# Performance work log

Hardware: AMD Instinct MI355X
Metric: run time of the kernel (lower is better)

The kernel has to match this reference:

```python
import jax, jax.numpy as jnp
import numpy as np

B, S, E, H = 4, 2048, 1024, 16
D = E // H  # head_dim = 64
MASK_VALUE = -10000.0


def setup_inputs() -> dict:
    key = jax.random.key(0)
    k1, k2, k3 = jax.random.split(key, 3)
    scale_qkv = 1.0 / np.sqrt(E)
    scale_out = 1.0 / np.sqrt(E)
    return {
        "x": jax.random.normal(k1, (B, S, E), dtype=jnp.float32),
        "w_qkv": jax.random.normal(k2, (E, 3 * E), dtype=jnp.float32) * scale_qkv,
        "b_qkv": jnp.zeros((3 * E,), dtype=jnp.float32),
        "w_out": jax.random.normal(k3, (E, E), dtype=jnp.float32) * scale_out,
        "b_out": jnp.zeros((E,), dtype=jnp.float32),
    }


def reference(x, w_qkv, b_qkv, w_out, b_out):
    # QKV projection (Dense with bias), then split into q, k, v
    qkv = x @ w_qkv + b_qkv                      # [B, S, 3E]
    q, k, v = jnp.split(qkv, 3, axis=2)          # each [B, S, E]

    def split_heads(t):
        return t.reshape(B, S, H, D).transpose(0, 2, 1, 3)  # [B, H, S, D]

    q, k, v = split_heads(q), split_heads(k), split_heads(v)

    # Scaled dot-product attention with causal mask (query_len == key_len == S)
    scores = jnp.einsum("bhqd,bhkd->bhqk", q, k) / jnp.sqrt(jnp.asarray(D, q.dtype))
    causal = jnp.tril(jnp.ones((S, S), dtype=bool))[None, None]  # [1,1,S,S]
    scores = jnp.where(causal, scores, MASK_VALUE)
    attn_weights = jax.nn.softmax(scores, axis=-1)               # [B,H,S,S]
    # attn dropout is deterministic (training=False) -> identity
    out = jnp.einsum("bhqk,bhkd->bhqd", attn_weights, v)         # [B,H,S,D]

    # Merge heads and output projection; resid dropout deterministic -> identity
    out = out.transpose(0, 2, 1, 3).reshape(B, S, E)
    out = out @ w_out + b_out
    return (out, attn_weights)
```

## Files before the change

### kernel.cpp

```cpp
#include <hip/hip_runtime.h>
#include <math.h>

typedef __attribute__((ext_vector_type(4))) float  f32x4;
typedef __attribute__((ext_vector_type(8))) __bf16 bf16x8;
typedef __attribute__((ext_vector_type(4))) __bf16 bf16x4;

constexpr int B_ = 4, S_ = 2048, E_ = 1024, H_ = 16, D_ = 64;
constexpr int M_ = B_ * S_;
constexpr int N3 = 3 * E_;

__device__ __forceinline__ f32x4 mfma16(bf16x8 a, bf16x8 b, f32x4 c) {
    return __builtin_amdgcn_mfma_f32_16x16x32_bf16(a, b, c, 0, 0, 0);
}
__device__ __forceinline__ void split2(float x, __bf16& h, __bf16& l) {
    h = (__bf16)x;
    l = (__bf16)(x - (float)h);
}

__device__ __forceinline__ void gemm_tile_core(
    const float* __restrict__ A, int lda,
    const float* __restrict__ Bm, int ldb,
    int K,
    __bf16* Ahi, __bf16* Alo, __bf16* Bhi, __bf16* Blo,
    f32x4 acc[4][4])
{
    const int tid  = threadIdx.x;
    const int lane = tid & 63;
    const int w    = tid >> 6;
    const int lr   = lane & 15;
    const int lq   = lane >> 4;
    const int wm   = w >> 1, wn = w & 1;

    for (int k0 = 0; k0 < K; k0 += 32) {
        __syncthreads();
#pragma unroll
        for (int i = 0; i < 2; ++i) {
            const int slot = tid + 256 * i;
            const int lr2 = slot & 15;
            const int lq2 = (slot >> 4) & 3;
            const int mi  = slot >> 6;
            const float* ap = A + (size_t)(mi * 16 + lr2) * lda + k0 + lq2 * 8;
            float4 a0 = *reinterpret_cast<const float4*>(ap);
            float4 a1 = *reinterpret_cast<const float4*>(ap + 4);
            float v8[8] = {a0.x, a0.y, a0.z, a0.w, a1.x, a1.y, a1.z, a1.w};
            bf16x8 hv, lv;
#pragma unroll
            for (int j = 0; j < 8; ++j) {
                __bf16 h0, l0;
                split2(v8[j], h0, l0);
                hv[j] = h0; lv[j] = l0;
            }
            *reinterpret_cast<bf16x8*>(Ahi + slot * 8) = hv;
            *reinterpret_cast<bf16x8*>(Alo + slot * 8) = lv;
        }
#pragma unroll
        for (int i = 0; i < 2; ++i) {
            const int slot = tid + 256 * i;
            const int lr2 = slot & 15;
            const int lq2 = (slot >> 4) & 3;
            const int ni  = slot >> 6;
            const float* bp = Bm + (size_t)(k0 + lq2 * 8) * ldb + ni * 16 + lr2;
            bf16x8 hv, lv;
#pragma unroll
            for (int j = 0; j < 8; ++j) {
                __bf16 h0, l0;
                split2(bp[(size_t)j * ldb], h0, l0);
                hv[j] = h0; lv[j] = l0;
            }
            *reinterpret_cast<bf16x8*>(Bhi + slot * 8) = hv;
            *reinterpret_cast<bf16x8*>(Blo + slot * 8) = lv;
        }
        __syncthreads();

        bf16x8 ah[4], al[4], bh[4], bl[4];
#pragma unroll
        for (int t = 0; t < 4; ++t) {
            const int sa = ((wm * 4 + t) * 4 + lq) * 16 + lr;
            ah[t] = *reinterpret_cast<const bf16x8*>(Ahi + sa * 8);
            al[t] = *reinterpret_cast<const bf16x8*>(Alo + sa * 8);
            const int sb = ((wn * 4 + t) * 4 + lq) * 16 + lr;
            bh[t] = *reinterpret_cast<const bf16x8*>(Bhi + sb * 8);
            bl[t] = *reinterpret_cast<const bf16x8*>(Blo + sb * 8);
        }
#pragma unroll
        for (int mi = 0; mi < 4; ++mi)
#pragma unroll
            for (int ni = 0; ni < 4; ++ni) {
                acc[mi][ni] = mfma16(ah[mi], bh[ni], acc[mi][ni]);
                acc[mi][ni] = mfma16(al[mi], bh[ni], acc[mi][ni]);
                acc[mi][ni] = mfma16(ah[mi], bl[ni], acc[mi][ni]);
            }
    }
}

__global__ __launch_bounds__(256, 2)
void qkv_kernel(const float* __restrict__ x, const float* __restrict__ wq,
                const float* __restrict__ bias,
                float* __restrict__ Qb, float* __restrict__ Kb,
                float* __restrict__ Vb) {
    __shared__ __align__(16) __bf16 Ahi[4096], Alo[4096];
    __shared__ __align__(16) __bf16 Bhi[4096], Blo[4096];

    const int bn = blockIdx.x * 128;
    const int bm = blockIdx.y * 128;
    const int tid  = threadIdx.x;
    const int lane = tid & 63;
    const int w    = tid >> 6;
    const int lr   = lane & 15;
    const int lq   = lane >> 4;
    const int wm   = w >> 1, wn = w & 1;

    f32x4 acc[4][4];
#pragma unroll
    for (int mi = 0; mi < 4; ++mi)
#pragma unroll
        for (int ni = 0; ni < 4; ++ni) acc[mi][ni] = (f32x4){0.f, 0.f, 0.f, 0.f};

    gemm_tile_core(x + (size_t)bm * E_, E_, wq + bn, N3, E_,
                   Ahi, Alo, Bhi, Blo, acc);

#pragma unroll
    for (int ni = 0; ni < 4; ++ni) {
        const int col  = bn + (wn * 4 + ni) * 16 + lr;
        const int t    = col >> 10;
        const int hcol = col & 1023;
        const int h    = hcol >> 6;
        const int d    = hcol & 63;
        float* dst = (t == 0) ? Qb : (t == 1) ? Kb : Vb;
        const float bv = bias[col];
#pragma unroll
        for (int mi = 0; mi < 4; ++mi) {
#pragma unroll
            for (int r = 0; r < 4; ++r) {
                const int row = bm + (wm * 4 + mi) * 16 + lq * 4 + r;
                const int b = row >> 11;
                const int s = row & 2047;
                dst[(((size_t)(b * H_ + h)) * S_ + s) * D_ + d] =
                    acc[mi][ni][r] + bv;
            }
        }
    }
}

__device__ __forceinline__ void stage_K(const float* __restrict__ src,
                                        __bf16* Khi, __bf16* Klo, int tid) {
    const int r0   = tid >> 4;
    const int c4   = (tid & 15) * 4;
    const int slot = (tid & 15) >> 1;
    const int half = (tid & 15) & 1;
#pragma unroll
    for (int i = 0; i < 4; ++i) {
        const int row = r0 + 16 * i;
        float4 v = *reinterpret_cast<const float4*>(&src[row * 64 + c4]);
        const int slotp = slot ^ (row & 7);
        const int idx = row * 64 + slotp * 8 + half * 4;
        bf16x4 hv, lv;
        __bf16 h0, l0;
        split2(v.x, h0, l0); hv[0] = h0; lv[0] = l0;
        split2(v.y, h0, l0); hv[1] = h0; lv[1] = l0;
        split2(v.z, h0, l0); hv[2] = h0; lv[2] = l0;
        split2(v.w, h0, l0); hv[3] = h0; lv[3] = l0;
        *reinterpret_cast<bf16x4*>(Khi + idx) = hv;
        *reinterpret_cast<bf16x4*>(Klo + idx) = lv;
    }
}

__device__ __forceinline__ void stage_V(const float* __restrict__ src,
                                        __bf16* Vhi, __bf16* Vlo, int tid) {
    const int kb  = tid >> 4;
    const int dq  = (tid & 15) * 4;
    const int kg  = kb >> 1;
    const int kc0 = (kb & 1) * 4;
    float rv[16];
#pragma unroll
    for (int i = 0; i < 4; ++i) {
        float4 t = *reinterpret_cast<const float4*>(&src[(kb * 4 + i) * 64 + dq]);
        rv[i * 4 + 0] = t.x; rv[i * 4 + 1] = t.y;
        rv[i * 4 + 2] = t.z; rv[i * 4 + 3] = t.w;
    }
#pragma unroll
    for (int di = 0; di < 4; ++di) {
        bf16x4 hv, lv;
        __bf16 h0, l0;
        split2(rv[0 * 4 + di], h0, l0); hv[0] = h0; lv[0] = l0;
        split2(rv[1 * 4 + di], h0, l0); hv[1] = h0; lv[1] = l0;
        split2(rv[2 * 4 + di], h0, l0); hv[2] = h0; lv[2] = l0;
        split2(rv[3 * 4 + di], h0, l0); hv[3] = h0; lv[3] = l0;
        const int idx = (kg * 64 + (dq + di)) * 8 + kc0;
        *reinterpret_cast<bf16x4*>(Vhi + idx) = hv;
        *reinterpret_cast<bf16x4*>(Vlo + idx) = lv;
    }
}

__device__ __forceinline__ void qk_tile(const __bf16* Khi, const __bf16* Klo,
                                        const bf16x8* qh, const bf16x8* ql,
                                        int lr, int lq, bool diag,
                                        int qrow0, int k0, f32x4 lg[4]) {
#pragma unroll
    for (int s = 0; s < 4; ++s) {
        f32x4 a = {0.f, 0.f, 0.f, 0.f};
        const int row = 16 * s + lr;
#pragma unroll
        for (int c = 0; c < 2; ++c) {
            const int slotp = (4 * c + lq) ^ (row & 7);
            bf16x8 kh = *reinterpret_cast<const bf16x8*>(Khi + row * 64 + slotp * 8);
            bf16x8 kl = *reinterpret_cast<const bf16x8*>(Klo + row * 64 + slotp * 8);
            a = mfma16(qh[c], kh, a);
            a = mfma16(ql[c], kh, a);
            a = mfma16(qh[c], kl, a);
        }
#pragma unroll
        for (int r = 0; r < 4; ++r) {
            float v = a[r] * 0.125f;
            if (diag && (k0 + 16 * s + lr) > (qrow0 + lq * 4 + r)) v = -1e30f;
            lg[s][r] = v;
        }
    }
}

__global__ __launch_bounds__(256, 3)
void attn_kernel(const float* __restrict__ Qg, const float* __restrict__ Kg,
                 const float* __restrict__ Vg, float* __restrict__ wts,
                 float* __restrict__ ctx) {
    __shared__ __align__(16) __bf16 Khi[4096];
    __shared__ __align__(16) __bf16 Klo[4096];
    __shared__ __align__(16) __bf16 Vhi[4096];
    __shared__ __align__(16) __bf16 Vlo[4096];
    __shared__ float sc[64][68];

    const int qt = blockIdx.x, h = blockIdx.y, b = blockIdx.z;
    const int q0 = qt * 64;
    const int tid = threadIdx.x;
    const int lane = tid & 63;
    const int w  = tid >> 6;
    const int lr = lane & 15;
    const int lq = lane >> 4;

    const size_t headbase = (size_t)(b * H_ + h) * S_ * D_;
    const float* Qp = Qg + headbase;
    const float* Kp = Kg + headbase;
    const float* Vp = Vg + headbase;
    float* wrow = wts + ((size_t)(b * H_ + h) * S_ + q0) * S_;

    bf16x8 qh[2], ql[2];
    {
        const int qrow = q0 + 16 * w + lr;
#pragma unroll
        for (int c = 0; c < 2; ++c) {
            const float* qp = &Qp[(size_t)qrow * D_ + c * 32 + lq * 8];
            float4 a  = *reinterpret_cast<const float4*>(qp);
            float4 bq = *reinterpret_cast<const float4*>(qp + 4);
            float v8[8] = {a.x, a.y, a.z, a.w, bq.x, bq.y, bq.z, bq.w};
#pragma unroll
            for (int j = 0; j < 8; ++j) {
                __bf16 h0, l0;
                split2(v8[j], h0, l0);
                qh[c][j] = h0; ql[c][j] = l0;
            }
        }
    }

    const int nkt = qt + 1;
    const int qrow0 = q0 + 16 * w;

    float m_run[4], l_run[4];
#pragma unroll
    for (int r = 0; r < 4; ++r) { m_run[r] = -INFINITY; l_run[r] = 0.f; }

    for (int kt = 0; kt < nkt; ++kt) {
        __syncthreads();
        stage_K(&Kp[(size_t)kt * 4096], Khi, Klo, tid);
        __syncthreads();
        f32x4 lg[4];
        qk_tile(Khi, Klo, qh, ql, lr, lq, kt == qt, qrow0, kt * 64, lg);
#pragma unroll
        for (int r = 0; r < 4; ++r) {
            float mx = fmaxf(fmaxf(lg[0][r], lg[1][r]), fmaxf(lg[2][r], lg[3][r]));
            mx = fmaxf(mx, __shfl_xor(mx, 1));
            mx = fmaxf(mx, __shfl_xor(mx, 2));
            mx = fmaxf(mx, __shfl_xor(mx, 4));
            mx = fmaxf(mx, __shfl_xor(mx, 8));
            const float mnew = fmaxf(m_run[r], mx);
            float ps = __expf(lg[0][r] - mnew) + __expf(lg[1][r] - mnew) +
                       __expf(lg[2][r] - mnew) + __expf(lg[3][r] - mnew);
            ps += __shfl_xor(ps, 1);
            ps += __shfl_xor(ps, 2);
            ps += __shfl_xor(ps, 4);
            ps += __shfl_xor(ps, 8);
            l_run[r] = l_run[r] * __expf(m_run[r] - mnew) + ps;
            m_run[r] = mnew;
        }
    }

    float linv[4];
#pragma unroll
    for (int r = 0; r < 4; ++r) linv[r] = 1.0f / l_run[r];

    f32x4 acc[4];
#pragma unroll
    for (int s = 0; s < 4; ++s) acc[s] = (f32x4){0.f, 0.f, 0.f, 0.f};

    for (int kt = 0; kt < nkt; ++kt) {
        __syncthreads();
        stage_K(&Kp[(size_t)kt * 4096], Khi, Klo, tid);
        stage_V(&Vp[(size_t)kt * 4096], Vhi, Vlo, tid);
        __syncthreads();

        f32x4 lg[4];
        qk_tile(Khi, Klo, qh, ql, lr, lq, kt == qt, qrow0, kt * 64, lg);
#pragma unroll
        for (int s = 0; s < 4; ++s)
#pragma unroll
            for (int r = 0; r < 4; ++r)
                sc[16 * w + lq * 4 + r][16 * s + lr] =
                    __expf(lg[s][r] - m_run[r]) * linv[r];
        __syncthreads();

        {
            const int c4 = (tid & 15) * 4;
            const int r0 = tid >> 4;
#pragma unroll
            for (int i = 0; i < 4; ++i) {
                const int row = r0 + 16 * i;
                float4 w4 = *reinterpret_cast<const float4*>(&sc[row][c4]);
                *reinterpret_cast<float4*>(
                    &wrow[(size_t)row * S_ + kt * 64 + c4]) = w4;
            }
        }

        bf16x8 pah[2], pal[2];
#pragma unroll
        for (int c = 0; c < 2; ++c) {
            const float* pr = &sc[16 * w + lr][lq * 8 + 32 * c];
            float4 p0 = *reinterpret_cast<const float4*>(pr);
            float4 p1 = *reinterpret_cast<const float4*>(pr + 4);
            float v8[8] = {p0.x, p0.y, p0.z, p0.w, p1.x, p1.y, p1.z, p1.w};
#pragma unroll
            for (int j = 0; j < 8; ++j) {
                __bf16 h0, l0;
                split2(v8[j], h0, l0);
                pah[c][j] = h0; pal[c][j] = l0;
            }
        }

#pragma unroll
        for (int s2 = 0; s2 < 4; ++s2) {
#pragma unroll
            for (int c = 0; c < 2; ++c) {
                const int kg = 4 * c + lq;
                const int d  = 16 * s2 + lr;
                bf16x8 vh = *reinterpret_cast<const bf16x8*>(Vhi + (kg * 64 + d) * 8);
                bf16x8 vl = *reinterpret_cast<const bf16x8*>(Vlo + (kg * 64 + d) * 8);
                acc[s2] = mfma16(pah[c], vh, acc[s2]);
                acc[s2] = mfma16(pah[c], vl, acc[s2]);
                acc[s2] = mfma16(pal[c], vh, acc[s2]);
            }
        }
    }

    {
        float4 z = {0.f, 0.f, 0.f, 0.f};
        const int c4 = (tid & 15) * 4;
        const int r0 = tid >> 4;
        for (int kt = nkt; kt < S_ / 64; ++kt) {
#pragma unroll
            for (int i = 0; i < 4; ++i) {
                const int row = r0 + 16 * i;
                *reinterpret_cast<float4*>(
                    &wrow[(size_t)row * S_ + kt * 64 + c4]) = z;
            }
        }
    }

#pragma unroll
    for (int s2 = 0; s2 < 4; ++s2)
#pragma unroll
        for (int r = 0; r < 4; ++r)
            ctx[((size_t)b * S_ + qrow0 + lq * 4 + r) * E_ + h * 64 + 16 * s2 + lr] =
                acc[s2][r];
}

__global__ __launch_bounds__(256, 2)
void proj_kernel(const float* __restrict__ ctx, const float* __restrict__ wo,
                 const float* __restrict__ bias, float* __restrict__ out) {
    __shared__ __align__(16) __bf16 Ahi[4096], Alo[4096];
    __shared__ __align__(16) __bf16 Bhi[4096], Blo[4096];

    const int bn = blockIdx.x * 128;
    const int bm = blockIdx.y * 128;
    const int tid  = threadIdx.x;
    const int lane = tid & 63;
    const int w    = tid >> 6;
    const int lr   = lane & 15;
    const int lq   = lane >> 4;
    const int wm   = w >> 1, wn = w & 1;

    f32x4 acc[4][4];
#pragma unroll
    for (int mi = 0; mi < 4; ++mi)
#pragma unroll
        for (int ni = 0; ni < 4; ++ni) acc[mi][ni] = (f32x4){0.f, 0.f, 0.f, 0.f};

    gemm_tile_core(ctx + (size_t)bm * E_, E_, wo + bn, E_, E_,
                   Ahi, Alo, Bhi, Blo, acc);

#pragma unroll
    for (int ni = 0; ni < 4; ++ni) {
        const int col = bn + (wn * 4 + ni) * 16 + lr;
        const float bv = bias[col];
#pragma unroll
        for (int mi = 0; mi < 4; ++mi) {
#pragma unroll
            for (int r = 0; r < 4; ++r) {
                const int row = bm + (wm * 4 + mi) * 16 + lq * 4 + r;
                out[(size_t)row * E_ + col] = acc[mi][ni][r] + bv;
            }
        }
    }
}

extern "C" void kernel_launch(void* const* d_in, const int* in_sizes, int n_in,
                              void* d_out, int out_size, void* d_ws,
                              size_t ws_size, hipStream_t stream) {
    (void)in_sizes; (void)n_in; (void)out_size; (void)ws_size;
    const float* x     = (const float*)d_in[0];
    const float* w_qkv = (const float*)d_in[1];
    const float* b_qkv = (const float*)d_in[2];
    const float* w_out = (const float*)d_in[3];
    const float* b_out = (const float*)d_in[4];

    float* out = (float*)d_out;
    float* wts = out + (size_t)M_ * E_;

    const size_t per = (size_t)B_ * H_ * S_ * D_;
    float* Qb  = (float*)d_ws;
    float* Kb  = Qb + per;
    float* Vb  = Kb + per;
    float* ctx = Vb + per;

    qkv_kernel<<<dim3(N3 / 128, M_ / 128), 256, 0, stream>>>(
        x, w_qkv, b_qkv, Qb, Kb, Vb);
    attn_kernel<<<dim3(S_ / 64, H_, B_), 256, 0, stream>>>(
        Qb, Kb, Vb, wts, ctx);
    proj_kernel<<<dim3(E_ / 128, M_ / 128), 256, 0, stream>>>(
        ctx, w_out, b_out, out);
}
```

Baseline: 1.730 ms.

## Pre-pack GEMM operands into tiled bf16 hi/lo buffers before the projection GEMMs

Adds separate pack kernels that split the fp32 activations and weights into bf16 hi/lo parts once, stored in the tile-ordered layout the MFMA loop reads. The QKV and output-projection GEMMs then copy contiguous pre-split tiles into shared memory instead of converting fp32 inside every block. Before, each A tile was re-split by every column block, and the B loads were strided column reads. In exchange the change adds four extra launches and extra global traffic for the packed buffers. The output-projection packed buffers reuse the Q workspace, which is safe only because the attention kernel has finished reading Q.

```diff
diff --git a/kernel.cpp b/kernel.cpp
--- a/kernel.cpp
+++ b/kernel.cpp
@@ -17,11 +17,60 @@
     l = (__bf16)(x - (float)h);
 }
 
-__device__ __forceinline__ void gemm_tile_core(
-    const float* __restrict__ A, int lda,
-    const float* __restrict__ Bm, int ldb,
-    int K,
-    __bf16* Ahi, __bf16* Alo, __bf16* Bhi, __bf16* Blo,
+__global__ __launch_bounds__(256)
+void pack_A_kernel(const float* __restrict__ A, int Kcols,
+                   ushort* __restrict__ hi, ushort* __restrict__ lo) {
+    const size_t idx = (size_t)blockIdx.x * 256 + threadIdx.x;
+    const int  slot = (int)(idx & 511);
+    const size_t pt = idx >> 9;
+    const int KT = Kcols >> 5;
+    const int kt = (int)(pt % KT);
+    const int p  = (int)(pt / KT);
+    const int lr2 = slot & 15, lq2 = (slot >> 4) & 3, mi = slot >> 6;
+    const float* ap = A + (size_t)(p * 128 + mi * 16 + lr2) * Kcols
+                        + kt * 32 + lq2 * 8;
+    float4 a0 = *reinterpret_cast<const float4*>(ap);
+    float4 a1 = *reinterpret_cast<const float4*>(ap + 4);
+    float v8[8] = {a0.x, a0.y, a0.z, a0.w, a1.x, a1.y, a1.z, a1.w};
+    bf16x8 hv, lv;
+#pragma unroll
+    for (int j = 0; j < 8; ++j) {
+        __bf16 h0, l0;
+        split2(v8[j], h0, l0);
+        hv[j] = h0; lv[j] = l0;
+    }
+    *reinterpret_cast<bf16x8*>(hi + idx * 8) = hv;
+    *reinterpret_cast<bf16x8*>(lo + idx * 8) = lv;
+}
+
+__global__ __launch_bounds__(256)
+void pack_B_kernel(const float* __restrict__ Bsrc, int Kdim, int Ncols,
+                   ushort* __restrict__ hi, ushort* __restrict__ lo) {
+    const size_t idx = (size_t)blockIdx.x * 256 + threadIdx.x;
+    const int  slot = (int)(idx & 511);
+    const size_t pt = idx >> 9;
+    const int KT = Kdim >> 5;
+    const int kt = (int)(pt % KT);
+    const int p  = (int)(pt / KT);
+    const int lr2 = slot & 15, lq2 = (slot >> 4) & 3, ni = slot >> 6;
+    const float* bp = Bsrc + (size_t)(kt * 32 + lq2 * 8) * Ncols
+                           + p * 128 + ni * 16 + lr2;
+    bf16x8 hv, lv;
+#pragma unroll
+    for (int j = 0; j < 8; ++j) {
+        __bf16 h0, l0;
+        split2(bp[(size_t)j * Ncols], h0, l0);
+        hv[j] = h0; lv[j] = l0;
+    }
+    *reinterpret_cast<bf16x8*>(hi + idx * 8) = hv;
+    *reinterpret_cast<bf16x8*>(lo + idx * 8) = lv;
+}
+
+__device__ __forceinline__ void gemm_packed_core(
+    const ushort* __restrict__ Ah, const ushort* __restrict__ Al,
+    const ushort* __restrict__ Bh, const ushort* __restrict__ Bl,
+    int KT,
+    __bf16* lAh, __bf16* lAl, __bf16* lBh, __bf16* lBl,
     f32x4 acc[4][4])
 {
     const int tid  = threadIdx.x;
@@ -31,44 +80,20 @@
     const int lq   = lane >> 4;
     const int wm   = w >> 1, wn = w & 1;
 
-    for (int k0 = 0; k0 < K; k0 += 32) {
-        __syncthreads();
+    for (int kt = 0; kt < KT; ++kt) {
+        __syncthreads();
+        const size_t toff = (size_t)kt * 4096;
 #pragma unroll
         for (int i = 0; i < 2; ++i) {
-            const int slot = tid + 256 * i;
-            const int lr2 = slot & 15;
-            const int lq2 = (slot >> 4) & 3;
-            const int mi  = slot >> 6;
-            const float* ap = A + (size_t)(mi * 16 + lr2) * lda + k0 + lq2 * 8;
-            float4 a0 = *reinterpret_cast<const float4*>(ap);
-            float4 a1 = *reinterpret_cast<const float4*>(ap + 4);
-            float v8[8] = {a0.x, a0.y, a0.z, a0.w, a1.x, a1.y, a1.z, a1.w};
-            bf16x8 hv, lv;
-#pragma unroll
-            for (int j = 0; j < 8; ++j) {
-                __bf16 h0, l0;
-                split2(v8[j], h0, l0);
-                hv[j] = h0; lv[j] = l0;
-            }
-            *reinterpret_cast<bf16x8*>(Ahi + slot * 8) = hv;
-            *reinterpret_cast<bf16x8*>(Alo + slot * 8) = lv;
-        }
-#pragma unroll
-        for (int i = 0; i < 2; ++i) {
-            const int slot = tid + 256 * i;
-            const int lr2 = slot & 15;
-            const int lq2 = (slot >> 4) & 3;
-            const int ni  = slot >> 6;
-            const float* bp = Bm + (size_t)(k0 + lq2 * 8) * ldb + ni * 16 + lr2;
-            bf16x8 hv, lv;
-#pragma unroll
-            for (int j = 0; j < 8; ++j) {
-                __bf16 h0, l0;
-                split2(bp[(size_t)j * ldb], h0, l0);
-                hv[j] = h0; lv[j] = l0;
-            }
-            *reinterpret_cast<bf16x8*>(Bhi + slot * 8) = hv;
-            *reinterpret_cast<bf16x8*>(Blo + slot * 8) = lv;
+            const int s = tid + 256 * i;
+            *reinterpret_cast<bf16x8*>(lAh + s * 8) =
+                *reinterpret_cast<const bf16x8*>(Ah + toff + s * 8);
+            *reinterpret_cast<bf16x8*>(lAl + s * 8) =
+                *reinterpret_cast<const bf16x8*>(Al + toff + s * 8);
+            *reinterpret_cast<bf16x8*>(lBh + s * 8) =
+                *reinterpret_cast<const bf16x8*>(Bh + toff + s * 8);
+            *reinterpret_cast<bf16x8*>(lBl + s * 8) =
+                *reinterpret_cast<const bf16x8*>(Bl + toff + s * 8);
         }
         __syncthreads();
 
@@ -76,11 +101,11 @@
 #pragma unroll
         for (int t = 0; t < 4; ++t) {
             const int sa = ((wm * 4 + t) * 4 + lq) * 16 + lr;
-            ah[t] = *reinterpret_cast<const bf16x8*>(Ahi + sa * 8);
-            al[t] = *reinterpret_cast<const bf16x8*>(Alo + sa * 8);
+            ah[t] = *reinterpret_cast<const bf16x8*>(lAh + sa * 8);
+            al[t] = *reinterpret_cast<const bf16x8*>(lAl + sa * 8);
             const int sb = ((wn * 4 + t) * 4 + lq) * 16 + lr;
-            bh[t] = *reinterpret_cast<const bf16x8*>(Bhi + sb * 8);
-            bl[t] = *reinterpret_cast<const bf16x8*>(Blo + sb * 8);
+            bh[t] = *reinterpret_cast<const bf16x8*>(lBh + sb * 8);
+            bl[t] = *reinterpret_cast<const bf16x8*>(lBl + sb * 8);
         }
 #pragma unroll
         for (int mi = 0; mi < 4; ++mi)
@@ -94,15 +119,18 @@
 }
 
 __global__ __launch_bounds__(256, 2)
-void qkv_kernel(const float* __restrict__ x, const float* __restrict__ wq,
+void qkv_kernel(const ushort* __restrict__ xh, const ushort* __restrict__ xl,
+                const ushort* __restrict__ wh, const ushort* __restrict__ wl,
                 const float* __restrict__ bias,
                 float* __restrict__ Qb, float* __restrict__ Kb,
                 float* __restrict__ Vb) {
-    __shared__ __align__(16) __bf16 Ahi[4096], Alo[4096];
-    __shared__ __align__(16) __bf16 Bhi[4096], Blo[4096];
-
-    const int bn = blockIdx.x * 128;
-    const int bm = blockIdx.y * 128;
+    __shared__ __align__(16) __bf16 lAh[4096], lAl[4096];
+    __shared__ __align__(16) __bf16 lBh[4096], lBl[4096];
+    constexpr int KT = E_ / 32;
+
+    const int pn = blockIdx.x;
+    const int pm = blockIdx.y;
+    const int bn = pn * 128, bm = pm * 128;
     const int tid  = threadIdx.x;
     const int lane = tid & 63;
     const int w    = tid >> 6;
@@ -116,8 +144,9 @@
 #pragma unroll
         for (int ni = 0; ni < 4; ++ni) acc[mi][ni] = (f32x4){0.f, 0.f, 0.f, 0.f};
 
-    gemm_tile_core(x + (size_t)bm * E_, E_, wq + bn, N3, E_,
-                   Ahi, Alo, Bhi, Blo, acc);
+    gemm_packed_core(xh + (size_t)pm * KT * 4096, xl + (size_t)pm * KT * 4096,
+                     wh + (size_t)pn * KT * 4096, wl + (size_t)pn * KT * 4096,
+                     KT, lAh, lAl, lBh, lBl, acc);
 
 #pragma unroll
     for (int ni = 0; ni < 4; ++ni) {
@@ -381,13 +410,16 @@
 }
 
 __global__ __launch_bounds__(256, 2)
-void proj_kernel(const float* __restrict__ ctx, const float* __restrict__ wo,
+void proj_kernel(const ushort* __restrict__ ch, const ushort* __restrict__ cl,
+                 const ushort* __restrict__ wh, const ushort* __restrict__ wl,
                  const float* __restrict__ bias, float* __restrict__ out) {
-    __shared__ __align__(16) __bf16 Ahi[4096], Alo[4096];
-    __shared__ __align__(16) __bf16 Bhi[4096], Blo[4096];
-
-    const int bn = blockIdx.x * 128;
-    const int bm = blockIdx.y * 128;
+    __shared__ __align__(16) __bf16 lAh[4096], lAl[4096];
+    __shared__ __align__(16) __bf16 lBh[4096], lBl[4096];
+    constexpr int KT = E_ / 32;
+
+    const int pn = blockIdx.x;
+    const int pm = blockIdx.y;
+    const int bn = pn * 128, bm = pm * 128;
     const int tid  = threadIdx.x;
     const int lane = tid & 63;
     const int w    = tid >> 6;
@@ -401,8 +433,9 @@
 #pragma unroll
         for (int ni = 0; ni < 4; ++ni) acc[mi][ni] = (f32x4){0.f, 0.f, 0.f, 0.f};
 
-    gemm_tile_core(ctx + (size_t)bm * E_, E_, wo + bn, E_, E_,
-                   Ahi, Alo, Bhi, Blo, acc);
+    gemm_packed_core(ch + (size_t)pm * KT * 4096, cl + (size_t)pm * KT * 4096,
+                     wh + (size_t)pn * KT * 4096, wl + (size_t)pn * KT * 4096,
+                     KT, lAh, lAl, lBh, lBl, acc);
 
 #pragma unroll
     for (int ni = 0; ni < 4; ++ni) {
@@ -438,10 +471,26 @@
     float* Vb  = Kb + per;
     float* ctx = Vb + per;
 
+    ushort* xh  = (ushort*)(ctx + per);
+    ushort* xl  = xh  + per;
+    ushort* wqh = xl  + per;
+    ushort* wql = wqh + (size_t)E_ * N3;
+    ushort* woh = wql + (size_t)E_ * N3;
+    ushort* wol = woh + (size_t)E_ * E_;
+    ushort* ch  = (ushort*)Qb;
+    ushort* cl  = ch + per;
+
+    pack_A_kernel<<<(M_ / 128) * (E_ / 32) * 2, 256, 0, stream>>>(x, E_, xh, xl);
+    pack_B_kernel<<<(N3 / 128) * (E_ / 32) * 2, 256, 0, stream>>>(
+        w_qkv, E_, N3, wqh, wql);
+    pack_B_kernel<<<(E_ / 128) * (E_ / 32) * 2, 256, 0, stream>>>(
+        w_out, E_, E_, woh, wol);
+
     qkv_kernel<<<dim3(N3 / 128, M_ / 128), 256, 0, stream>>>(
-        x, w_qkv, b_qkv, Qb, Kb, Vb);
+        xh, xl, wqh, wql, b_qkv, Qb, Kb, Vb);
     attn_kernel<<<dim3(S_ / 64, H_, B_), 256, 0, stream>>>(
         Qb, Kb, Vb, wts, ctx);
+    pack_A_kernel<<<(M_ / 128) * (E_ / 32) * 2, 256, 0, stream>>>(ctx, E_, ch, cl);
     proj_kernel<<<dim3(E_ / 128, M_ / 128), 256, 0, stream>>>(
-        ctx, w_out, b_out, out);
-}
+        ch, cl, woh, wol, b_out, out);
+}
```

After: 1.817 ms. 5.0% more time.
